# Performance work log

Measured on AMD Instinct MI355X. Metric: run time of the kernel, lower is better.

The kernel has to match this reference:

```python
import jax, jax.numpy as jnp
import numpy as np

B, T, D = 4, 2048, 1024
H, HD = 16, 64          # heads, head_dim
F = 2 * HD              # hedgehog feature dim
C = 64                  # chunk size (fla fused_chunk)
EPS = 1e-5


def setup_inputs() -> dict:
    key = jax.random.key(0)
    ks = jax.random.split(key, 8)
    s = 0.02
    return {
        "hidden_states": jax.random.normal(ks[0], (B, T, D), jnp.float32),
        "residual": jax.random.normal(ks[1], (B, T, D), jnp.float32),
        "norm_weight": jnp.ones((D,), jnp.float32),
        "w_q": jax.random.normal(ks[2], (D, D), jnp.float32) * s,
        "w_k": jax.random.normal(ks[3], (D, D), jnp.float32) * s,
        "w_v": jax.random.normal(ks[4], (D, D), jnp.float32) * s,
        "w_o": jax.random.normal(ks[5], (D, D), jnp.float32) * s,
        "hh_q_w": jnp.eye(HD, dtype=jnp.float32) + 0.01 * jax.random.normal(ks[6], (HD, HD), jnp.float32),
        "hh_q_b": jnp.zeros((HD,), jnp.float32),
        "hh_k_w": jnp.eye(HD, dtype=jnp.float32) + 0.01 * jax.random.normal(ks[7], (HD, HD), jnp.float32),
        "hh_k_b": jnp.zeros((HD,), jnp.float32),
    }


def _rmsnorm(x, w):
    var = jnp.mean(jnp.square(x), axis=-1, keepdims=True)
    return x * jax.lax.rsqrt(var + EPS) * w


def _hedgehog(x, w, b):
    # x: [B,H,T,HD]; learned linear then softmax over cat([y, -y])
    y = jnp.einsum('bhtd,ed->bhte', x, w) + b
    return jax.nn.softmax(jnp.concatenate([y, -y], axis=-1), axis=-1)  # [B,H,T,2*HD]


def reference(hidden_states, residual, norm_weight, w_q, w_k, w_v, w_o,
              hh_q_w, hh_q_b, hh_k_w, hh_k_b):
    # fused add + RMSNorm, prenorm, residual kept in fp32
    resid = (hidden_states + residual).astype(jnp.float32)
    x = _rmsnorm(resid, norm_weight).astype(hidden_states.dtype)

    def proj(w):  # [B,T,D] @ [D,D] -> [B,H,T,HD]
        return (x @ w).reshape(B, T, H, HD).transpose(0, 2, 1, 3)

    q = _hedgehog(proj(w_q), hh_q_w, hh_q_b)            # [B,H,T,F]
    k = _hedgehog(proj(w_k), hh_k_w, hh_k_b)            # [B,H,T,F]
    v = proj(w_v)                                        # [B,H,T,HD]
    q = q * (F ** -0.5)

    # chunked causal linear attention: o_t = phi(q_t) . sum_{s<=t} phi(k_s) v_s^T
    N = T // C
    qc = q.reshape(B, H, N, C, F)
    kc = k.reshape(B, H, N, C, F)
    vc = v.reshape(B, H, N, C, HD)

    kv = jnp.einsum('bhncf,bhncd->bhnfd', kc, vc)        # per-chunk state update
    S = jnp.cumsum(kv, axis=2)
    S_excl = jnp.concatenate([jnp.zeros_like(S[:, :, :1]), S[:, :, :-1]], axis=2)
    inter = jnp.einsum('bhncf,bhnfd->bhncd', qc, S_excl)

    scores = jnp.einsum('bhncf,bhnmf->bhncm', qc, kc)    # intra-chunk [C,C]
    tri = jnp.tril(jnp.ones((C, C), dtype=bool))
    scores = jnp.where(tri, scores, 0.0)
    intra = jnp.einsum('bhncm,bhnmd->bhncd', scores, vc)

    o = (inter + intra).reshape(B, H, T, HD).transpose(0, 2, 1, 3).reshape(B, T, D)
    o = o @ w_o
    return o, resid
```

## Files before the change

kernel.cpp:

```cpp
#include <hip/hip_runtime.h>
#include <math.h>

#define B_   4
#define T_   2048
#define D_   1024
#define H_   16
#define HD_  64
#define F_   128
#define C_   64
#define NCH  32
#define BT_  8192
#define BTD_ 8388608

typedef __bf16 bf16_t;
typedef __bf16 bf16x4 __attribute__((ext_vector_type(4)));
typedef __bf16 bf16x8 __attribute__((ext_vector_type(8)));
typedef float  f32x4  __attribute__((ext_vector_type(4)));

#define GLD16(gp, lp)                                                      \
  __builtin_amdgcn_global_load_lds(                                       \
      (const __attribute__((address_space(1))) unsigned int*)(const void*)(gp), \
      (__attribute__((address_space(3))) unsigned int*)(void*)(lp), 16, 0, 0)

__global__ __launch_bounds__(256) void k_transpose_all(
    const float* __restrict__ w_q, const float* __restrict__ w_k,
    const float* __restrict__ w_v, const float* __restrict__ w_o,
    bf16_t* __restrict__ wqkvT, bf16_t* __restrict__ woT) {
  const int z = blockIdx.z;
  const float* w = (z == 0) ? w_q : (z == 1) ? w_k : (z == 2) ? w_v : w_o;
  bf16_t* wT = (z < 3) ? (wqkvT + (size_t)z * D_ * D_) : woT;
  __shared__ float tile[64][65];
  const int tid = threadIdx.x;
  const int n0 = blockIdx.x * 64;
  const int k0 = blockIdx.y * 64;
#pragma unroll
  for (int g = 0; g < 4; ++g) {
    const int k = g * 16 + (tid >> 4);
    float4 v = *(const float4*)(w + (size_t)(k0 + k) * D_ + n0 + (tid & 15) * 4);
    tile[k][(tid & 15) * 4 + 0] = v.x;
    tile[k][(tid & 15) * 4 + 1] = v.y;
    tile[k][(tid & 15) * 4 + 2] = v.z;
    tile[k][(tid & 15) * 4 + 3] = v.w;
  }
  __syncthreads();
#pragma unroll
  for (int g = 0; g < 4; ++g) {
    const int n = g * 16 + (tid >> 4);
    bf16x4 o;
#pragma unroll
    for (int i = 0; i < 4; ++i) o[i] = (__bf16)tile[(tid & 15) * 4 + i][n];
    *(bf16x4*)(wT + (size_t)(n0 + n) * D_ + k0 + (tid & 15) * 4) = o;
  }
}

__global__ __launch_bounds__(256) void k_add_rmsnorm(
    const float* __restrict__ hs, const float* __restrict__ res,
    const float* __restrict__ w, float* __restrict__ resid_out,
    bf16_t* __restrict__ x_out) {
  const int row = blockIdx.x;
  const size_t base = (size_t)row * D_;
  const int tid = threadIdx.x;
  float4 h4 = *(const float4*)(hs + base + tid * 4);
  float4 r4 = *(const float4*)(res + base + tid * 4);
  float4 s4;
  s4.x = h4.x + r4.x; s4.y = h4.y + r4.y;
  s4.z = h4.z + r4.z; s4.w = h4.w + r4.w;
  *(float4*)(resid_out + base + tid * 4) = s4;
  float ss = s4.x * s4.x + s4.y * s4.y + s4.z * s4.z + s4.w * s4.w;
#pragma unroll
  for (int off = 32; off > 0; off >>= 1) ss += __shfl_down(ss, off);
  __shared__ float red[4];
  if ((tid & 63) == 0) red[tid >> 6] = ss;
  __syncthreads();
  const float tot = red[0] + red[1] + red[2] + red[3];
  const float rstd = rsqrtf(tot * (1.0f / D_) + 1e-5f);
  float4 w4 = *(const float4*)(w + tid * 4);
  bf16x4 xo;
  xo[0] = (__bf16)(s4.x * rstd * w4.x);
  xo[1] = (__bf16)(s4.y * rstd * w4.y);
  xo[2] = (__bf16)(s4.z * rstd * w4.z);
  xo[3] = (__bf16)(s4.w * rstd * w4.w);
  *(bf16x4*)(x_out + base + tid * 4) = xo;
}

template <int F32OUT>
__global__ __launch_bounds__(256) void k_gemm_mfma(
    const bf16_t* __restrict__ A, const bf16_t* __restrict__ BTb,
    void* __restrict__ Cb) {
  __shared__ bf16_t As[128 * 32];
  __shared__ bf16_t Bs[128 * 32];
  const int z = blockIdx.z;
  const bf16_t* BT = BTb + (size_t)z * (D_ * D_);
  const int tid = threadIdx.x;
  const int lane = tid & 63;
  const int wave = tid >> 6;
  const int bm = (blockIdx.x * 8 + (blockIdx.y & 7)) * 128;
  const int bn = (blockIdx.y >> 3) * 128;
  const int wm = (wave >> 1) * 64;
  const int wn = (wave & 1) * 64;
  const int srow = wave * 32 + (lane >> 2);
  const int scol = (lane & 3) * 8;
  const bf16_t* ag0 = A + (size_t)(bm + srow) * D_ + scol;
  const bf16_t* ag1 = A + (size_t)(bm + srow + 16) * D_ + scol;
  const bf16_t* bg0 = BT + (size_t)(bn + srow) * D_ + scol;
  const bf16_t* bg1 = BT + (size_t)(bn + srow + 16) * D_ + scol;
  bf16_t* lA0 = As + wave * 1024;
  bf16_t* lA1 = As + wave * 1024 + 512;
  bf16_t* lB0 = Bs + wave * 1024;
  bf16_t* lB1 = Bs + wave * 1024 + 512;
  const int frow = lane & 15;
  const int fks = (lane >> 4) * 8;

  f32x4 acc[4][4] = {};
  for (int k0 = 0; k0 < D_; k0 += 32) {
    __syncthreads();
    GLD16(ag0 + k0, lA0);
    GLD16(ag1 + k0, lA1);
    GLD16(bg0 + k0, lB0);
    GLD16(bg1 + k0, lB1);
    __syncthreads();
    bf16x8 af[4], bq[4];
#pragma unroll
    for (int i = 0; i < 4; ++i) {
      af[i] = *(const bf16x8*)(&As[(wm + i * 16 + frow) * 32 + fks]);
      bq[i] = *(const bf16x8*)(&Bs[(wn + i * 16 + frow) * 32 + fks]);
    }
#pragma unroll
    for (int i = 0; i < 4; ++i)
#pragma unroll
      for (int j = 0; j < 4; ++j)
        acc[i][j] = __builtin_amdgcn_mfma_f32_16x16x32_bf16(af[i], bq[j],
                                                            acc[i][j], 0, 0, 0);
  }

  const int crow0 = bm + wm + (lane >> 4) * 4;
  const int ccol0 = bn + wn + (lane & 15);
#pragma unroll
  for (int i = 0; i < 4; ++i)
#pragma unroll
    for (int j = 0; j < 4; ++j) {
      const size_t rb = (size_t)(crow0 + i * 16) * D_ + ccol0 + j * 16;
#pragma unroll
      for (int r = 0; r < 4; ++r) {
        if (F32OUT)
          ((float*)Cb)[rb + (size_t)r * D_] = acc[i][j][r];
        else
          ((bf16_t*)Cb + (size_t)z * ((size_t)BT_ * D_))[rb + (size_t)r * D_] =
              (__bf16)acc[i][j][r];
      }
    }
}

__global__ __launch_bounds__(256) void k_hedgehog_mfma(
    const bf16_t* __restrict__ pq, const bf16_t* __restrict__ pk,
    const float* __restrict__ wq, const float* __restrict__ wk,
    const float* __restrict__ bq, const float* __restrict__ bk,
    bf16_t* __restrict__ outq, bf16_t* __restrict__ outk) {
  const int z = blockIdx.y;
  const bf16_t* p = z ? pk : pq;
  const float* w = z ? wk : wq;
  const float* bias = z ? bk : bq;
  bf16_t* out = z ? outk : outq;
  const float scale = z ? 1.0f : 0.08838834764831845f;

  const int blk = blockIdx.x;
  const int n = blk % NCH;
  const int h = (blk / NCH) % H_;
  const int b = blk / (NCH * H_);
  const int tid = threadIdx.x;
  const int lane = tid & 63;
  const int wv = tid >> 6;
  const int l15 = lane & 15;
  const int lhi = lane >> 4;

  const int trowA = n * 64 + wv * 16 + l15;
  bf16x8 pa[2];
#pragma unroll
  for (int s = 0; s < 2; ++s)
    pa[s] = *(const bf16x8*)(p + (size_t)(b * T_ + trowA) * D_ + h * 64 +
                             s * 32 + lhi * 8);

  f32x4 acc[4] = {};
#pragma unroll
  for (int j = 0; j < 4; ++j) {
#pragma unroll
    for (int s = 0; s < 2; ++s) {
      const float* wr = w + (16 * j + l15) * 64 + s * 32 + lhi * 8;
      float4 w0 = *(const float4*)(wr);
      float4 w1 = *(const float4*)(wr + 4);
      bf16x8 wb;
      wb[0] = (__bf16)w0.x; wb[1] = (__bf16)w0.y;
      wb[2] = (__bf16)w0.z; wb[3] = (__bf16)w0.w;
      wb[4] = (__bf16)w1.x; wb[5] = (__bf16)w1.y;
      wb[6] = (__bf16)w1.z; wb[7] = (__bf16)w1.w;
      acc[j] = __builtin_amdgcn_mfma_f32_16x16x32_bf16(pa[s], wb, acc[j], 0, 0, 0);
    }
  }
  float be[4];
#pragma unroll
  for (int j = 0; j < 4; ++j) be[j] = bias[16 * j + l15];

  const int trowC = n * 64 + wv * 16 + lhi * 4;
#pragma unroll
  for (int r = 0; r < 4; ++r) {
    float y[4];
#pragma unroll
    for (int j = 0; j < 4; ++j) y[j] = acc[j][r] + be[j];
    float m = fmaxf(fmaxf(fabsf(y[0]), fabsf(y[1])),
                    fmaxf(fabsf(y[2]), fabsf(y[3])));
#pragma unroll
    for (int o = 1; o < 16; o <<= 1) m = fmaxf(m, __shfl_xor(m, o));
    float e1[4], e2[4], s = 0.f;
#pragma unroll
    for (int j = 0; j < 4; ++j) {
      e1[j] = expf(y[j] - m);
      e2[j] = expf(-y[j] - m);
      s += e1[j] + e2[j];
    }
#pragma unroll
    for (int o = 1; o < 16; o <<= 1) s += __shfl_xor(s, o);
    const float inv = scale / s;
    bf16_t* ob = out + ((size_t)(b * H_ + h) * T_ + trowC + r) * F_;
#pragma unroll
    for (int j = 0; j < 4; ++j) {
      ob[16 * j + l15] = (__bf16)(e1[j] * inv);
      ob[64 + 16 * j + l15] = (__bf16)(e2[j] * inv);
    }
  }
}

__global__ __launch_bounds__(256) void k_chunk_kv(
    const bf16_t* __restrict__ kf,
    const bf16_t* __restrict__ pv,
    bf16_t* __restrict__ kvout) {
  __shared__ bf16_t kt[128 * 64];
  __shared__ bf16_t vt[64 * 64];
  const int blk = blockIdx.x;
  const int n = blk % NCH;
  const int h = (blk / NCH) % H_;
  const int b = blk / (NCH * H_);
  const int tid = threadIdx.x;
  const bf16_t* kb = kf + ((size_t)(b * H_ + h) * T_ + n * 64) * F_;
#pragma unroll
  for (int g = 0; g < 4; ++g) {
    int i8 = g * 256 + tid;
    int c = i8 >> 4, f8 = (i8 & 15) * 8;
    bf16x8 v8 = *(const bf16x8*)(kb + (size_t)c * F_ + f8);
#pragma unroll
    for (int jj = 0; jj < 8; ++jj) {
      int f = f8 + jj;
      kt[f * 64 + (c ^ ((f & 7) << 3))] = v8[jj];
    }
  }
#pragma unroll
  for (int g = 0; g < 2; ++g) {
    int i8 = g * 256 + tid;
    int m = i8 >> 3, d8 = (i8 & 7) * 8;
    bf16x8 v8 = *(const bf16x8*)(pv + (size_t)(b * T_ + n * 64 + m) * D_ +
                                 h * 64 + d8);
#pragma unroll
    for (int jj = 0; jj < 8; ++jj) {
      int d = d8 + jj;
      vt[d * 64 + (m ^ ((d & 7) << 3))] = v8[jj];
    }
  }
  __syncthreads();
  const int lane = tid & 63, wv = tid >> 6;
  const int l15 = lane & 15, lhi = lane >> 4;
  const int drow = wv * 16 + l15;
  f32x4 acc[8] = {};
#pragma unroll
  for (int s = 0; s < 2; ++s) {
    const int c0 = s * 32 + lhi * 8;
    bf16x8 va = *(const bf16x8*)(vt + drow * 64 + (c0 ^ ((drow & 7) << 3)));
#pragma unroll
    for (int j = 0; j < 8; ++j) {
      const int frow = j * 16 + l15;
      bf16x8 ka = *(const bf16x8*)(kt + frow * 64 + (c0 ^ ((frow & 7) << 3)));
      acc[j] = __builtin_amdgcn_mfma_f32_16x16x32_bf16(va, ka, acc[j], 0, 0, 0);
    }
  }
  bf16_t* ob = kvout + (size_t)blk * 8192;
#pragma unroll
  for (int j = 0; j < 8; ++j)
#pragma unroll
    for (int r = 0; r < 4; ++r) {
      int d = wv * 16 + lhi * 4 + r, f = j * 16 + l15;
      ob[d * 128 + f] = (__bf16)acc[j][r];
    }
}

__global__ __launch_bounds__(256) void k_cumsum_excl(bf16_t* __restrict__ kv) {
  const int bh = blockIdx.x >> 3;
  const int slice = blockIdx.x & 7;
  const int e = slice * 1024 + threadIdx.x * 4;
  bf16_t* base = kv + (size_t)bh * NCH * 8192 + e;
  bf16x4 vals[NCH];
#pragma unroll
  for (int n = 0; n < NCH; ++n) vals[n] = *(const bf16x4*)(base + (size_t)n * 8192);
  float run[4] = {0.f, 0.f, 0.f, 0.f};
#pragma unroll
  for (int n = 0; n < NCH; ++n) {
    bf16x4 o;
#pragma unroll
    for (int j = 0; j < 4; ++j) {
      o[j] = (__bf16)run[j];
      run[j] += (float)vals[n][j];
    }
    *(bf16x4*)(base + (size_t)n * 8192) = o;
  }
}

__global__ __launch_bounds__(256) void k_attn_chunk(
    const bf16_t* __restrict__ qf,
    const bf16_t* __restrict__ kf,
    const bf16_t* __restrict__ pv,
    const bf16_t* __restrict__ kvx,
    bf16_t* __restrict__ o_tmp) {
  __shared__ bf16_t scs[64 * 64];
  __shared__ bf16_t vt[64 * 64];
  const int blk = blockIdx.x;
  const int n = blk % NCH;
  const int h = (blk / NCH) % H_;
  const int b = blk / (NCH * H_);
  const int tid = threadIdx.x;
#pragma unroll
  for (int g = 0; g < 2; ++g) {
    int i8 = g * 256 + tid;
    int m = i8 >> 3, d8 = (i8 & 7) * 8;
    bf16x8 v8 = *(const bf16x8*)(pv + (size_t)(b * T_ + n * 64 + m) * D_ +
                                 h * 64 + d8);
#pragma unroll
    for (int jj = 0; jj < 8; ++jj) {
      int d = d8 + jj;
      vt[d * 64 + (m ^ ((d & 7) << 3))] = v8[jj];
    }
  }
  const int lane = tid & 63, wv = tid >> 6;
  const int l15 = lane & 15, lhi = lane >> 4;
  const size_t rowbase = (size_t)(b * H_ + h) * T_ + n * 64;
  const bf16_t* qb = qf + rowbase * F_;
  const bf16_t* kb = kf + rowbase * F_;

  bf16x8 qa[4];
#pragma unroll
  for (int s = 0; s < 4; ++s)
    qa[s] = *(const bf16x8*)(qb + (wv * 16 + l15) * F_ + s * 32 + lhi * 8);

  f32x4 accS[4] = {};
#pragma unroll
  for (int j = 0; j < 4; ++j)
#pragma unroll
    for (int s = 0; s < 4; ++s) {
      bf16x8 kk = *(const bf16x8*)(kb + (j * 16 + l15) * F_ + s * 32 + lhi * 8);
      accS[j] = __builtin_amdgcn_mfma_f32_16x16x32_bf16(qa[s], kk, accS[j], 0, 0, 0);
    }
#pragma unroll
  for (int j = 0; j < 4; ++j)
#pragma unroll
    for (int r = 0; r < 4; ++r) {
      int c = wv * 16 + lhi * 4 + r;
      int m = j * 16 + l15;
      float v = (m <= c) ? accS[j][r] : 0.f;
      scs[c * 64 + (m ^ ((c & 7) << 3))] = (__bf16)v;
    }

  f32x4 acc[4] = {};
  const bf16_t* kvb = kvx + (size_t)blk * 8192;
#pragma unroll
  for (int j = 0; j < 4; ++j)
#pragma unroll
    for (int s = 0; s < 4; ++s) {
      bf16x8 sv = *(const bf16x8*)(kvb + (j * 16 + l15) * 128 + s * 32 + lhi * 8);
      acc[j] = __builtin_amdgcn_mfma_f32_16x16x32_bf16(qa[s], sv, acc[j], 0, 0, 0);
    }

  __syncthreads();

  const int crow = wv * 16 + l15;
#pragma unroll
  for (int s2 = 0; s2 < 2; ++s2) {
    const int m0 = s2 * 32 + lhi * 8;
    bf16x8 sa = *(const bf16x8*)(scs + crow * 64 + (m0 ^ ((crow & 7) << 3)));
#pragma unroll
    for (int j = 0; j < 4; ++j) {
      const int dr = j * 16 + l15;
      bf16x8 vb = *(const bf16x8*)(vt + dr * 64 + (m0 ^ ((dr & 7) << 3)));
      acc[j] = __builtin_amdgcn_mfma_f32_16x16x32_bf16(sa, vb, acc[j], 0, 0, 0);
    }
  }

#pragma unroll
  for (int j = 0; j < 4; ++j)
#pragma unroll
    for (int r = 0; r < 4; ++r) {
      int c = wv * 16 + lhi * 4 + r, d = j * 16 + l15;
      o_tmp[(size_t)(b * T_ + n * 64 + c) * D_ + h * 64 + d] = (__bf16)acc[j][r];
    }
}

extern "C" void kernel_launch(void* const* d_in, const int* in_sizes, int n_in,
                              void* d_out, int out_size, void* d_ws, size_t ws_size,
                              hipStream_t stream) {
  const float* hs   = (const float*)d_in[0];
  const float* res  = (const float*)d_in[1];
  const float* nw   = (const float*)d_in[2];
  const float* w_q  = (const float*)d_in[3];
  const float* w_k  = (const float*)d_in[4];
  const float* w_v  = (const float*)d_in[5];
  const float* w_o  = (const float*)d_in[6];
  const float* hhqw = (const float*)d_in[7];
  const float* hhqb = (const float*)d_in[8];
  const float* hhkw = (const float*)d_in[9];
  const float* hhkb = (const float*)d_in[10];

  float* out       = (float*)d_out;
  float* o_final   = out;
  float* resid_out = out + BTD_;

  char* wsb = (char*)d_ws;
  bf16_t* x_bf  = (bf16_t*)(wsb);
  bf16_t* wqkvT = (bf16_t*)(wsb + (16ull << 20));
  bf16_t* woT   = (bf16_t*)(wsb + (22ull << 20));
  bf16_t* qf    = (bf16_t*)(wsb + (24ull << 20));
  bf16_t* kf    = (bf16_t*)(wsb + (56ull << 20));
  bf16_t* pqkv  = (bf16_t*)(wsb + (88ull << 20));
  bf16_t* pq    = pqkv;
  bf16_t* pk    = pqkv + (size_t)BTD_;
  bf16_t* pvb   = pqkv + (size_t)2 * BTD_;
  bf16_t* kv    = pqkv;
  bf16_t* o_tmp = x_bf;

  k_transpose_all<<<dim3(16, 16, 4), 256, 0, stream>>>(w_q, w_k, w_v, w_o,
                                                       wqkvT, woT);

  k_add_rmsnorm<<<BT_, 256, 0, stream>>>(hs, res, nw, resid_out, x_bf);

  k_gemm_mfma<0><<<dim3(8, 64, 3), 256, 0, stream>>>(x_bf, wqkvT, (void*)pqkv);

  k_hedgehog_mfma<<<dim3(2048, 2), 256, 0, stream>>>(pq, pk, hhqw, hhkw,
                                                     hhqb, hhkb, qf, kf);

  k_chunk_kv<<<2048, 256, 0, stream>>>(kf, pvb, kv);
  k_cumsum_excl<<<512, 256, 0, stream>>>(kv);
  k_attn_chunk<<<2048, 256, 0, stream>>>(qf, kf, pvb, kv, o_tmp);

  k_gemm_mfma<1><<<dim3(8, 64, 1), 256, 0, stream>>>(o_tmp, woT, (void*)o_final);
}
```

Measured before the change: 347.4 us.

## Fuse hedgehog with chunk KV, double-buffer GEMM LDS, stage attention inputs in LDS

Several unrelated changes at once. The GEMM now double-buffers its LDS tiles with a swizzled layout so the next K-slice loads while the current one computes, with one barrier per iteration instead of two. The hedgehog kernel now also computes the per-chunk k^T v state from its own feature tile, which removes the separate chunk_kv kernel and its re-read of kf. Q/K stores are staged through a transposed LDS tile for vector writes, and the hedgehog weights are pre-converted to bf16 in the transpose kernel. The cumsum uses wider vectors, and the attention kernel stages K and the KV state into swizzled LDS with async loads; the larger LDS footprints may lower occupancy.

After: 299.6 us. 1.16x faster.

```diff
diff --git a/kernel.cpp b/kernel.cpp
--- a/kernel.cpp
+++ b/kernel.cpp
@@ -25,12 +25,23 @@
 __global__ __launch_bounds__(256) void k_transpose_all(
     const float* __restrict__ w_q, const float* __restrict__ w_k,
     const float* __restrict__ w_v, const float* __restrict__ w_o,
-    bf16_t* __restrict__ wqkvT, bf16_t* __restrict__ woT) {
+    const float* __restrict__ hhqw, const float* __restrict__ hhkw,
+    bf16_t* __restrict__ wqkvT, bf16_t* __restrict__ woT,
+    bf16_t* __restrict__ hhbf) {
   const int z = blockIdx.z;
+  const int tid = threadIdx.x;
+  if (z == 4) {
+    const int gid = blockIdx.y * 16 + blockIdx.x;
+    if (gid < 32) {
+      const int i = gid * 256 + tid;
+      const float v = (i < 4096) ? hhqw[i] : hhkw[i - 4096];
+      hhbf[i] = (__bf16)v;
+    }
+    return;
+  }
   const float* w = (z == 0) ? w_q : (z == 1) ? w_k : (z == 2) ? w_v : w_o;
   bf16_t* wT = (z < 3) ? (wqkvT + (size_t)z * D_ * D_) : woT;
   __shared__ float tile[64][65];
-  const int tid = threadIdx.x;
   const int n0 = blockIdx.x * 64;
   const int k0 = blockIdx.y * 64;
 #pragma unroll
@@ -87,8 +98,8 @@
 __global__ __launch_bounds__(256) void k_gemm_mfma(
     const bf16_t* __restrict__ A, const bf16_t* __restrict__ BTb,
     void* __restrict__ Cb) {
-  __shared__ bf16_t As[128 * 32];
-  __shared__ bf16_t Bs[128 * 32];
+  __shared__ bf16_t As[2][128 * 32];
+  __shared__ bf16_t Bs[2][128 * 32];
   const int z = blockIdx.z;
   const bf16_t* BT = BTb + (size_t)z * (D_ * D_);
   const int tid = threadIdx.x;
@@ -98,32 +109,41 @@
   const int bn = (blockIdx.y >> 3) * 128;
   const int wm = (wave >> 1) * 64;
   const int wn = (wave & 1) * 64;
-  const int srow = wave * 32 + (lane >> 2);
-  const int scol = (lane & 3) * 8;
-  const bf16_t* ag0 = A + (size_t)(bm + srow) * D_ + scol;
-  const bf16_t* ag1 = A + (size_t)(bm + srow + 16) * D_ + scol;
-  const bf16_t* bg0 = BT + (size_t)(bn + srow) * D_ + scol;
-  const bf16_t* bg1 = BT + (size_t)(bn + srow + 16) * D_ + scol;
-  bf16_t* lA0 = As + wave * 1024;
-  bf16_t* lA1 = As + wave * 1024 + 512;
-  bf16_t* lB0 = Bs + wave * 1024;
-  bf16_t* lB1 = Bs + wave * 1024 + 512;
+  const int r0 = wave * 32 + (lane >> 2);
+  const int ssw = (((lane >> 2) & 3) ^ (lane >> 4));
+  const int scol = (((lane & 3) ^ ssw) << 3);
+  const bf16_t* ap0 = A + (size_t)(bm + r0) * D_ + scol;
+  const bf16_t* ap1 = A + (size_t)(bm + r0 + 16) * D_ + scol;
+  const bf16_t* bp0 = BT + (size_t)(bn + r0) * D_ + scol;
+  const bf16_t* bp1 = BT + (size_t)(bn + r0 + 16) * D_ + scol;
+  const int lb0 = wave * 1024;
+  const int lb1 = wave * 1024 + 512;
   const int frow = lane & 15;
-  const int fks = (lane >> 4) * 8;
+  const int lhi = lane >> 4;
+  const int rsw = ((frow & 3) ^ ((frow >> 2) & 3));
+  const int rcol = ((lhi ^ rsw) << 3);
 
   f32x4 acc[4][4] = {};
+  GLD16(ap0, &As[0][lb0]);
+  GLD16(ap1, &As[0][lb1]);
+  GLD16(bp0, &Bs[0][lb0]);
+  GLD16(bp1, &Bs[0][lb1]);
+  __syncthreads();
+
   for (int k0 = 0; k0 < D_; k0 += 32) {
-    __syncthreads();
-    GLD16(ag0 + k0, lA0);
-    GLD16(ag1 + k0, lA1);
-    GLD16(bg0 + k0, lB0);
-    GLD16(bg1 + k0, lB1);
-    __syncthreads();
+    const int cur = (k0 >> 5) & 1;
+    if (k0 + 32 < D_) {
+      const int nxt = cur ^ 1;
+      GLD16(ap0 + k0 + 32, &As[nxt][lb0]);
+      GLD16(ap1 + k0 + 32, &As[nxt][lb1]);
+      GLD16(bp0 + k0 + 32, &Bs[nxt][lb0]);
+      GLD16(bp1 + k0 + 32, &Bs[nxt][lb1]);
+    }
     bf16x8 af[4], bq[4];
 #pragma unroll
     for (int i = 0; i < 4; ++i) {
-      af[i] = *(const bf16x8*)(&As[(wm + i * 16 + frow) * 32 + fks]);
-      bq[i] = *(const bf16x8*)(&Bs[(wn + i * 16 + frow) * 32 + fks]);
+      af[i] = *(const bf16x8*)(&As[cur][(wm + i * 16 + frow) * 32 + rcol]);
+      bq[i] = *(const bf16x8*)(&Bs[cur][(wn + i * 16 + frow) * 32 + rcol]);
     }
 #pragma unroll
     for (int i = 0; i < 4; ++i)
@@ -131,6 +151,7 @@
       for (int j = 0; j < 4; ++j)
         acc[i][j] = __builtin_amdgcn_mfma_f32_16x16x32_bf16(af[i], bq[j],
                                                             acc[i][j], 0, 0, 0);
+    __syncthreads();
   }
 
   const int crow0 = bm + wm + (lane >> 4) * 4;
@@ -151,14 +172,20 @@
     }
 }
 
-__global__ __launch_bounds__(256) void k_hedgehog_mfma(
+__device__ __forceinline__ int swF(int f) { return (f & 7) ^ ((f >> 3) & 7); }
+
+__global__ __launch_bounds__(256) void k_hedgehog_kv(
     const bf16_t* __restrict__ pq, const bf16_t* __restrict__ pk,
-    const float* __restrict__ wq, const float* __restrict__ wk,
+    const bf16_t* __restrict__ hhbf,
     const float* __restrict__ bq, const float* __restrict__ bk,
-    bf16_t* __restrict__ outq, bf16_t* __restrict__ outk) {
+    const bf16_t* __restrict__ pv,
+    bf16_t* __restrict__ outq, bf16_t* __restrict__ outk,
+    bf16_t* __restrict__ kvout) {
+  __shared__ bf16_t featT[128 * 64];
+  __shared__ bf16_t vt[64 * 64];
   const int z = blockIdx.y;
   const bf16_t* p = z ? pk : pq;
-  const float* w = z ? wk : wq;
+  const bf16_t* wb = hhbf + z * 4096;
   const float* bias = z ? bk : bq;
   bf16_t* out = z ? outk : outq;
   const float scale = z ? 1.0f : 0.08838834764831845f;
@@ -173,34 +200,39 @@
   const int l15 = lane & 15;
   const int lhi = lane >> 4;
 
+  if (z) {
+#pragma unroll
+    for (int g = 0; g < 2; ++g) {
+      int i8 = g * 256 + tid;
+      int m = i8 >> 3, d8 = (i8 & 7) * 8;
+      bf16x8 v8 = *(const bf16x8*)(pv + (size_t)(b * T_ + n * 64 + m) * D_ +
+                                   h * 64 + d8);
+#pragma unroll
+      for (int jj = 0; jj < 8; ++jj) {
+        int d = d8 + jj;
+        vt[d * 64 + (m ^ ((d & 7) << 3))] = v8[jj];
+      }
+    }
+  }
+
   const int trowA = n * 64 + wv * 16 + l15;
   bf16x8 pa[2];
 #pragma unroll
   for (int s = 0; s < 2; ++s)
     pa[s] = *(const bf16x8*)(p + (size_t)(b * T_ + trowA) * D_ + h * 64 +
                              s * 32 + lhi * 8);
-
   f32x4 acc[4] = {};
 #pragma unroll
-  for (int j = 0; j < 4; ++j) {
+  for (int j = 0; j < 4; ++j)
 #pragma unroll
     for (int s = 0; s < 2; ++s) {
-      const float* wr = w + (16 * j + l15) * 64 + s * 32 + lhi * 8;
-      float4 w0 = *(const float4*)(wr);
-      float4 w1 = *(const float4*)(wr + 4);
-      bf16x8 wb;
-      wb[0] = (__bf16)w0.x; wb[1] = (__bf16)w0.y;
-      wb[2] = (__bf16)w0.z; wb[3] = (__bf16)w0.w;
-      wb[4] = (__bf16)w1.x; wb[5] = (__bf16)w1.y;
-      wb[6] = (__bf16)w1.z; wb[7] = (__bf16)w1.w;
-      acc[j] = __builtin_amdgcn_mfma_f32_16x16x32_bf16(pa[s], wb, acc[j], 0, 0, 0);
-    }
-  }
+      bf16x8 wf = *(const bf16x8*)(wb + (16 * j + l15) * 64 + s * 32 + lhi * 8);
+      acc[j] = __builtin_amdgcn_mfma_f32_16x16x32_bf16(pa[s], wf, acc[j], 0, 0, 0);
+    }
   float be[4];
 #pragma unroll
   for (int j = 0; j < 4; ++j) be[j] = bias[16 * j + l15];
 
-  const int trowC = n * 64 + wv * 16 + lhi * 4;
 #pragma unroll
   for (int r = 0; r < 4; ++r) {
     float y[4];
@@ -213,101 +245,81 @@
     float e1[4], e2[4], s = 0.f;
 #pragma unroll
     for (int j = 0; j < 4; ++j) {
-      e1[j] = expf(y[j] - m);
-      e2[j] = expf(-y[j] - m);
+      e1[j] = __expf(y[j] - m);
+      e2[j] = __expf(-y[j] - m);
       s += e1[j] + e2[j];
     }
 #pragma unroll
     for (int o = 1; o < 16; o <<= 1) s += __shfl_xor(s, o);
     const float inv = scale / s;
-    bf16_t* ob = out + ((size_t)(b * H_ + h) * T_ + trowC + r) * F_;
+    const int c = wv * 16 + lhi * 4 + r;
 #pragma unroll
     for (int j = 0; j < 4; ++j) {
-      ob[16 * j + l15] = (__bf16)(e1[j] * inv);
-      ob[64 + 16 * j + l15] = (__bf16)(e2[j] * inv);
-    }
-  }
-}
-
-__global__ __launch_bounds__(256) void k_chunk_kv(
-    const bf16_t* __restrict__ kf,
-    const bf16_t* __restrict__ pv,
-    bf16_t* __restrict__ kvout) {
-  __shared__ bf16_t kt[128 * 64];
-  __shared__ bf16_t vt[64 * 64];
-  const int blk = blockIdx.x;
-  const int n = blk % NCH;
-  const int h = (blk / NCH) % H_;
-  const int b = blk / (NCH * H_);
-  const int tid = threadIdx.x;
-  const bf16_t* kb = kf + ((size_t)(b * H_ + h) * T_ + n * 64) * F_;
+      const int f1 = 16 * j + l15, f2 = f1 + 64;
+      featT[f1 * 64 + (((c >> 3) ^ swF(f1)) << 3) + (c & 7)] = (__bf16)(e1[j] * inv);
+      featT[f2 * 64 + (((c >> 3) ^ swF(f2)) << 3) + (c & 7)] = (__bf16)(e2[j] * inv);
+    }
+  }
+  __syncthreads();
+
+  const size_t obase = (size_t)(b * H_ + h) * T_ + n * 64;
 #pragma unroll
   for (int g = 0; g < 4; ++g) {
     int i8 = g * 256 + tid;
-    int c = i8 >> 4, f8 = (i8 & 15) * 8;
-    bf16x8 v8 = *(const bf16x8*)(kb + (size_t)c * F_ + f8);
+    int t = i8 >> 4, fc = i8 & 15;
+    bf16x8 o8;
 #pragma unroll
     for (int jj = 0; jj < 8; ++jj) {
-      int f = f8 + jj;
-      kt[f * 64 + (c ^ ((f & 7) << 3))] = v8[jj];
-    }
-  }
-#pragma unroll
-  for (int g = 0; g < 2; ++g) {
-    int i8 = g * 256 + tid;
-    int m = i8 >> 3, d8 = (i8 & 7) * 8;
-    bf16x8 v8 = *(const bf16x8*)(pv + (size_t)(b * T_ + n * 64 + m) * D_ +
-                                 h * 64 + d8);
-#pragma unroll
-    for (int jj = 0; jj < 8; ++jj) {
-      int d = d8 + jj;
-      vt[d * 64 + (m ^ ((d & 7) << 3))] = v8[jj];
-    }
-  }
-  __syncthreads();
-  const int lane = tid & 63, wv = tid >> 6;
-  const int l15 = lane & 15, lhi = lane >> 4;
-  const int drow = wv * 16 + l15;
-  f32x4 acc[8] = {};
-#pragma unroll
-  for (int s = 0; s < 2; ++s) {
-    const int c0 = s * 32 + lhi * 8;
-    bf16x8 va = *(const bf16x8*)(vt + drow * 64 + (c0 ^ ((drow & 7) << 3)));
+      int f = fc * 8 + jj;
+      o8[jj] = featT[f * 64 + (((t >> 3) ^ swF(f)) << 3) + (t & 7)];
+    }
+    *(bf16x8*)(out + (obase + t) * F_ + fc * 8) = o8;
+  }
+
+  if (z) {
+    const int drow = wv * 16 + l15;
+    f32x4 a2[8] = {};
+#pragma unroll
+    for (int s = 0; s < 2; ++s) {
+      const int c0 = s * 32 + lhi * 8;
+      bf16x8 va = *(const bf16x8*)(vt + drow * 64 + (c0 ^ ((drow & 7) << 3)));
+#pragma unroll
+      for (int j = 0; j < 8; ++j) {
+        const int fr = j * 16 + l15;
+        bf16x8 kb = *(const bf16x8*)(featT + fr * 64 +
+                                     ((((c0 >> 3) ^ swF(fr))) << 3));
+        a2[j] = __builtin_amdgcn_mfma_f32_16x16x32_bf16(va, kb, a2[j], 0, 0, 0);
+      }
+    }
+    bf16_t* ob = kvout + (size_t)blk * 8192;
+#pragma unroll
+    for (int j = 0; j < 8; ++j)
+#pragma unroll
+      for (int r = 0; r < 4; ++r) {
+        int d = wv * 16 + lhi * 4 + r, f = j * 16 + l15;
+        ob[d * 128 + f] = (__bf16)a2[j][r];
+      }
+  }
+}
+
+__global__ __launch_bounds__(256) void k_cumsum_excl(bf16_t* __restrict__ kv) {
+  const int bh = blockIdx.x >> 2;
+  const int slice = blockIdx.x & 3;
+  const int e = slice * 2048 + threadIdx.x * 8;
+  bf16_t* base = kv + (size_t)bh * NCH * 8192 + e;
+  bf16x8 vals[NCH];
+#pragma unroll
+  for (int n = 0; n < NCH; ++n) vals[n] = *(const bf16x8*)(base + (size_t)n * 8192);
+  float run[8] = {};
+#pragma unroll
+  for (int n = 0; n < NCH; ++n) {
+    bf16x8 o;
 #pragma unroll
     for (int j = 0; j < 8; ++j) {
-      const int frow = j * 16 + l15;
-      bf16x8 ka = *(const bf16x8*)(kt + frow * 64 + (c0 ^ ((frow & 7) << 3)));
-      acc[j] = __builtin_amdgcn_mfma_f32_16x16x32_bf16(va, ka, acc[j], 0, 0, 0);
-    }
-  }
-  bf16_t* ob = kvout + (size_t)blk * 8192;
-#pragma unroll
-  for (int j = 0; j < 8; ++j)
-#pragma unroll
-    for (int r = 0; r < 4; ++r) {
-      int d = wv * 16 + lhi * 4 + r, f = j * 16 + l15;
-      ob[d * 128 + f] = (__bf16)acc[j][r];
-    }
-}
-
-__global__ __launch_bounds__(256) void k_cumsum_excl(bf16_t* __restrict__ kv) {
-  const int bh = blockIdx.x >> 3;
-  const int slice = blockIdx.x & 7;
-  const int e = slice * 1024 + threadIdx.x * 4;
-  bf16_t* base = kv + (size_t)bh * NCH * 8192 + e;
-  bf16x4 vals[NCH];
-#pragma unroll
-  for (int n = 0; n < NCH; ++n) vals[n] = *(const bf16x4*)(base + (size_t)n * 8192);
-  float run[4] = {0.f, 0.f, 0.f, 0.f};
-#pragma unroll
-  for (int n = 0; n < NCH; ++n) {
-    bf16x4 o;
-#pragma unroll
-    for (int j = 0; j < 4; ++j) {
       o[j] = (__bf16)run[j];
       run[j] += (float)vals[n][j];
     }
-    *(bf16x4*)(base + (size_t)n * 8192) = o;
+    *(bf16x8*)(base + (size_t)n * 8192) = o;
   }
 }
 
@@ -317,13 +329,33 @@
     const bf16_t* __restrict__ pv,
     const bf16_t* __restrict__ kvx,
     bf16_t* __restrict__ o_tmp) {
+  __shared__ bf16_t kt[64 * 128];
+  __shared__ bf16_t st[64 * 128];
+  __shared__ bf16_t vt[64 * 64];
   __shared__ bf16_t scs[64 * 64];
-  __shared__ bf16_t vt[64 * 64];
   const int blk = blockIdx.x;
   const int n = blk % NCH;
   const int h = (blk / NCH) % H_;
   const int b = blk / (NCH * H_);
   const int tid = threadIdx.x;
+  const int lane = tid & 63;
+  const int wv = tid >> 6;
+  const int l15 = lane & 15;
+  const int lhi = lane >> 4;
+  const size_t rowbase = (size_t)(b * H_ + h) * T_ + n * 64;
+  const bf16_t* qb = qf + rowbase * F_;
+  const bf16_t* kb = kf + rowbase * F_;
+  const bf16_t* kvb = kvx + (size_t)blk * 8192;
+
+#pragma unroll
+  for (int g = 0; g < 4; ++g) {
+    const int cl = g * 256 + tid;
+    const int row = cl >> 4, pc = cl & 15;
+    const int cc = pc ^ (row & 7);
+    const int lb = (g * 256 + wv * 64) * 8;
+    GLD16(kb + (size_t)row * F_ + cc * 8, kt + lb);
+    GLD16(kvb + (size_t)row * F_ + cc * 8, st + lb);
+  }
 #pragma unroll
   for (int g = 0; g < 2; ++g) {
     int i8 = g * 256 + tid;
@@ -336,25 +368,24 @@
       vt[d * 64 + (m ^ ((d & 7) << 3))] = v8[jj];
     }
   }
-  const int lane = tid & 63, wv = tid >> 6;
-  const int l15 = lane & 15, lhi = lane >> 4;
-  const size_t rowbase = (size_t)(b * H_ + h) * T_ + n * 64;
-  const bf16_t* qb = qf + rowbase * F_;
-  const bf16_t* kb = kf + rowbase * F_;
-
   bf16x8 qa[4];
 #pragma unroll
   for (int s = 0; s < 4; ++s)
     qa[s] = *(const bf16x8*)(qb + (wv * 16 + l15) * F_ + s * 32 + lhi * 8);
 
+  __syncthreads();
+
   f32x4 accS[4] = {};
 #pragma unroll
-  for (int j = 0; j < 4; ++j)
+  for (int j = 0; j < 4; ++j) {
+    const int tr = j * 16 + l15;
 #pragma unroll
     for (int s = 0; s < 4; ++s) {
-      bf16x8 kk = *(const bf16x8*)(kb + (j * 16 + l15) * F_ + s * 32 + lhi * 8);
+      bf16x8 kk = *(const bf16x8*)(kt + tr * 128 +
+                                   (((s * 4 + lhi) ^ (tr & 7)) << 3));
       accS[j] = __builtin_amdgcn_mfma_f32_16x16x32_bf16(qa[s], kk, accS[j], 0, 0, 0);
     }
+  }
 #pragma unroll
   for (int j = 0; j < 4; ++j)
 #pragma unroll
@@ -366,16 +397,16 @@
     }
 
   f32x4 acc[4] = {};
-  const bf16_t* kvb = kvx + (size_t)blk * 8192;
-#pragma unroll
-  for (int j = 0; j < 4; ++j)
+#pragma unroll
+  for (int j = 0; j < 4; ++j) {
+    const int dr = j * 16 + l15;
 #pragma unroll
     for (int s = 0; s < 4; ++s) {
-      bf16x8 sv = *(const bf16x8*)(kvb + (j * 16 + l15) * 128 + s * 32 + lhi * 8);
+      bf16x8 sv = *(const bf16x8*)(st + dr * 128 +
+                                   (((s * 4 + lhi) ^ (dr & 7)) << 3));
       acc[j] = __builtin_amdgcn_mfma_f32_16x16x32_bf16(qa[s], sv, acc[j], 0, 0, 0);
     }
-
-  __syncthreads();
+  }
 
   const int crow = wv * 16 + l15;
 #pragma unroll
@@ -428,21 +459,22 @@
   bf16_t* pq    = pqkv;
   bf16_t* pk    = pqkv + (size_t)BTD_;
   bf16_t* pvb   = pqkv + (size_t)2 * BTD_;
-  bf16_t* kv    = pqkv;
+  bf16_t* kv    = (bf16_t*)(wsb + (136ull << 20));
+  bf16_t* hhbf  = (bf16_t*)(wsb + (168ull << 20));
   bf16_t* o_tmp = x_bf;
 
-  k_transpose_all<<<dim3(16, 16, 4), 256, 0, stream>>>(w_q, w_k, w_v, w_o,
-                                                       wqkvT, woT);
+  k_transpose_all<<<dim3(16, 16, 5), 256, 0, stream>>>(
+      w_q, w_k, w_v, w_o, hhqw, hhkw, wqkvT, woT, hhbf);
 
   k_add_rmsnorm<<<BT_, 256, 0, stream>>>(hs, res, nw, resid_out, x_bf);
 
   k_gemm_mfma<0><<<dim3(8, 64, 3), 256, 0, stream>>>(x_bf, wqkvT, (void*)pqkv);
 
-  k_hedgehog_mfma<<<dim3(2048, 2), 256, 0, stream>>>(pq, pk, hhqw, hhkw,
-                                                     hhqb, hhkb, qf, kf);
-
-  k_chunk_kv<<<2048, 256, 0, stream>>>(kf, pvb, kv);
-  k_cumsum_excl<<<512, 256, 0, stream>>>(kv);
+  k_hedgehog_kv<<<dim3(2048, 2), 256, 0, stream>>>(pq, pk, hhbf, hhqb, hhkb,
+                                                   pvb, qf, kf, kv);
+
+  k_cumsum_excl<<<256, 256, 0, stream>>>(kv);
+
   k_attn_chunk<<<2048, 256, 0, stream>>>(qf, kf, pvb, kv, o_tmp);
 
   k_gemm_mfma<1><<<dim3(8, 64, 1), 256, 0, stream>>>(o_tmp, woT, (void*)o_final);
```
